# Performance work log

Hardware: AMD Instinct MI355X
Metric: run time of the kernel (lower is better)

The kernel has to match this reference:

```python
import jax, jax.numpy as jnp
import numpy as np

B, T, HOR = 128, 512, 64
M, Q, DFF = 1, 5, 7
D_IN = DFF + M            # 8
H = 512                   # d_hidden
NL = 2                    # n_layers
G = 4 * H                 # gate dim


def _cell(x, h, c, w_ih, w_hh, b):
    # PyTorch LSTM cell: gates ordered i, f, g, o
    g = x @ w_ih.T + h @ w_hh.T + b
    i, f, gg, o = jnp.split(g, 4, axis=-1)
    c = jax.nn.sigmoid(f) * c + jax.nn.sigmoid(i) * jnp.tanh(gg)
    h = jax.nn.sigmoid(o) * jnp.tanh(c)
    return h, c


def _bidi_layer(xs, w_ih, w_hh, b):
    # xs: [T, B, Din]; w_ih: [2, 4H, Din]; returns concat outputs and final states
    bsz = xs.shape[1]
    h0 = jnp.zeros((bsz, H), xs.dtype)

    def run(dirn, reverse):
        def step(carry, xt):
            h, c = carry
            h, c = _cell(xt, h, c, w_ih[dirn], w_hh[dirn], b[dirn])
            return (h, c), h
        (hT, cT), ys = jax.lax.scan(step, (h0, h0), xs, reverse=reverse)
        return ys, hT, cT

    ys_f, hf, cf = run(0, False)
    ys_b, hb, cb = run(1, True)
    return jnp.concatenate([ys_f, ys_b], axis=-1), (hf, hb, cf, cb)


def setup_inputs() -> dict:
    key = jax.random.key(0)
    ks = iter(jax.random.split(key, 24))
    s = 0.05
    inp = {
        "X": jax.random.normal(next(ks), (B, T, D_IN), jnp.float32),
        "future_features": jax.random.normal(next(ks), (B, HOR, DFF), jnp.float32),
        "Y_teacher": jax.random.normal(next(ks), (B, HOR, M), jnp.float32),
        "horizon_span": HOR,
        "enc_w_ih_l0": s * jax.random.normal(next(ks), (2, G, D_IN), jnp.float32),
        "enc_w_hh_l0": s * jax.random.normal(next(ks), (2, G, H), jnp.float32),
        "enc_b_l0": s * jax.random.normal(next(ks), (2, G), jnp.float32),
        "enc_w_ih_l1": s * jax.random.normal(next(ks), (2, G, 2 * H), jnp.float32),
        "enc_w_hh_l1": s * jax.random.normal(next(ks), (2, G, H), jnp.float32),
        "enc_b_l1": s * jax.random.normal(next(ks), (2, G), jnp.float32),
        "dec_w_ih_l0": s * jax.random.normal(next(ks), (G, D_IN), jnp.float32),
        "dec_w_hh_l0": s * jax.random.normal(next(ks), (G, H), jnp.float32),
        "dec_b_l0": s * jax.random.normal(next(ks), (G,), jnp.float32),
        "dec_w_ih_l1": s * jax.random.normal(next(ks), (G, H), jnp.float32),
        "dec_w_hh_l1": s * jax.random.normal(next(ks), (G, H), jnp.float32),
        "dec_b_l1": s * jax.random.normal(next(ks), (G,), jnp.float32),
        "w_bidi_h": s * jax.random.normal(next(ks), (NL * H, 2 * NL * H), jnp.float32),
        "b_bidi_h": s * jax.random.normal(next(ks), (NL * H,), jnp.float32),
        "w_out": s * jax.random.normal(next(ks), (M * Q, H), jnp.float32),
        "b_out": s * jax.random.normal(next(ks), (M * Q,), jnp.float32),
    }
    return inp


def reference(X, future_features, Y_teacher, horizon_span,
              enc_w_ih_l0, enc_w_hh_l0, enc_b_l0,
              enc_w_ih_l1, enc_w_hh_l1, enc_b_l1,
              dec_w_ih_l0, dec_w_hh_l0, dec_b_l0,
              dec_w_ih_l1, dec_w_hh_l1, dec_b_l1,
              w_bidi_h, b_bidi_h, w_out, b_out):
    bsz = X.shape[0]
    xs = jnp.swapaxes(X, 0, 1)  # [T, B, D_IN]

    ys1, (hf0, hb0, cf0, cb0) = _bidi_layer(xs, enc_w_ih_l0, enc_w_hh_l0, enc_b_l0)
    _,   (hf1, hb1, cf1, cb1) = _bidi_layer(ys1, enc_w_ih_l1, enc_w_hh_l1, enc_b_l1)

    # merge bidirectional final states: layout [B, (layer0 fwd|bwd, layer1 fwd|bwd)]
    h_flat = jnp.concatenate([hf0, hb0, hf1, hb1], axis=-1)  # [B, 2*NL*H]
    c_flat = jnp.concatenate([cf0, cb0, cf1, cb1], axis=-1)
    # NOTE: original module (faithfully) uses the *h* projection + ELU for c too
    h_m = jax.nn.elu(h_flat @ w_bidi_h.T + b_bidi_h).reshape(bsz, NL, H)
    c_m = jax.nn.elu(c_flat @ w_bidi_h.T + b_bidi_h).reshape(bsz, NL, H)

    futs = jnp.swapaxes(future_features, 0, 1)  # [HOR, B, DFF]
    inp_y0 = X[:, -1, :M]                        # [B, M]

    def step(carry, f_t):
        inp_y, h0, c0, h1, c1 = carry
        x = jnp.concatenate([inp_y, f_t], axis=-1)          # [B, D_IN]
        h0, c0 = _cell(x, h0, c0, dec_w_ih_l0, dec_w_hh_l0, dec_b_l0)
        h1, c1 = _cell(h0, h1, c1, dec_w_ih_l1, dec_w_hh_l1, dec_b_l1)
        y = h1 @ w_out.T + b_out                             # [B, M*Q]
        return (y[:, :M], h0, c0, h1, c1), y

    carry0 = (inp_y0, h_m[:, 0], c_m[:, 0], h_m[:, 1], c_m[:, 1])
    _, ys = jax.lax.scan(step, carry0, futs)                 # [HOR, B, M*Q]
    out = jnp.swapaxes(ys, 0, 1).reshape(bsz, horizon_span, M, Q)
    return out
```

## Files before the change

### kernel.cpp

```cpp
#include <hip/hip_runtime.h>
#include <hip/hip_bf16.h>
#include <cstddef>
#include <cstdint>


typedef __attribute__((ext_vector_type(8))) short short8;
typedef __attribute__((ext_vector_type(4))) float f32x4;

__device__ __forceinline__ float sigm_(float x) { return 1.0f / (1.0f + __expf(-x)); }

struct MProb {
  const __hip_bfloat16* A;
  const float* bpk;
  const __hip_bfloat16* S0;
  const __hip_bfloat16* S1;
  const float* cin;
  float* cout;
  __hip_bfloat16* hT;
  float* hf32;
  int ld0, ld1, ldh;
};

template<int N0, int N1, int KT, bool FIRST, bool WF32>
__global__ __launch_bounds__(256) void k_mcell(MProb P0, MProb P1)
{
  const MProb P = (blockIdx.x >= 32) ? P1 : P0;
  const int m0  = (blockIdx.x & 31) * 64;
  const int tid = threadIdx.x;
  const int lane = tid & 63;
  const int w  = tid >> 6;
  const int wm = w >> 1, wn = w & 1;
  const int r = lane & 15, q = lane >> 4;

  f32x4 acc[2][4];
#pragma unroll
  for (int am = 0; am < 2; ++am)
#pragma unroll
    for (int bn = 0; bn < 4; ++bn) acc[am][bn] = (f32x4){0.f, 0.f, 0.f, 0.f};

  const short* Ab = (const short*)P.A + (size_t)(m0 + wm * 32 + r) * KT + q * 8;

  if constexpr (!FIRST) {
    const short* Bb = (const short*)P.S0 + (size_t)(wn * 64 + r) * P.ld0 + q * 8;
    const size_t bs = (size_t)16 * P.ld0;
#pragma unroll 4
    for (int kk = 0; kk < N0; ++kk) {
      short8 a0 = *(const short8*)(Ab + kk * 32);
      short8 a1 = *(const short8*)(Ab + (size_t)16 * KT + kk * 32);
      short8 b0 = *(const short8*)(Bb + kk * 32);
      short8 b1 = *(const short8*)(Bb + kk * 32 + bs);
      short8 b2 = *(const short8*)(Bb + kk * 32 + 2 * bs);
      short8 b3 = *(const short8*)(Bb + kk * 32 + 3 * bs);
      acc[0][0] = __builtin_amdgcn_mfma_f32_16x16x32_bf16(a0, b0, acc[0][0], 0, 0, 0);
      acc[0][1] = __builtin_amdgcn_mfma_f32_16x16x32_bf16(a0, b1, acc[0][1], 0, 0, 0);
      acc[0][2] = __builtin_amdgcn_mfma_f32_16x16x32_bf16(a0, b2, acc[0][2], 0, 0, 0);
      acc[0][3] = __builtin_amdgcn_mfma_f32_16x16x32_bf16(a0, b3, acc[0][3], 0, 0, 0);
      acc[1][0] = __builtin_amdgcn_mfma_f32_16x16x32_bf16(a1, b0, acc[1][0], 0, 0, 0);
      acc[1][1] = __builtin_amdgcn_mfma_f32_16x16x32_bf16(a1, b1, acc[1][1], 0, 0, 0);
      acc[1][2] = __builtin_amdgcn_mfma_f32_16x16x32_bf16(a1, b2, acc[1][2], 0, 0, 0);
      acc[1][3] = __builtin_amdgcn_mfma_f32_16x16x32_bf16(a1, b3, acc[1][3], 0, 0, 0);
    }
  }
  {
    const short* Bb = (const short*)P.S1 + (size_t)(wn * 64 + r) * P.ld1 + q * 8;
    const size_t bs = (size_t)16 * P.ld1;
#pragma unroll 4
    for (int kk = 0; kk < N1; ++kk) {
      short8 a0 = *(const short8*)(Ab + (size_t)(N0 + kk) * 32);
      short8 a1 = *(const short8*)(Ab + (size_t)16 * KT + (size_t)(N0 + kk) * 32);
      short8 b0 = *(const short8*)(Bb + kk * 32);
      short8 b1 = *(const short8*)(Bb + kk * 32 + bs);
      short8 b2 = *(const short8*)(Bb + kk * 32 + 2 * bs);
      short8 b3 = *(const short8*)(Bb + kk * 32 + 3 * bs);
      acc[0][0] = __builtin_amdgcn_mfma_f32_16x16x32_bf16(a0, b0, acc[0][0], 0, 0, 0);
      acc[0][1] = __builtin_amdgcn_mfma_f32_16x16x32_bf16(a0, b1, acc[0][1], 0, 0, 0);
      acc[0][2] = __builtin_amdgcn_mfma_f32_16x16x32_bf16(a0, b2, acc[0][2], 0, 0, 0);
      acc[0][3] = __builtin_amdgcn_mfma_f32_16x16x32_bf16(a0, b3, acc[0][3], 0, 0, 0);
      acc[1][0] = __builtin_amdgcn_mfma_f32_16x16x32_bf16(a1, b0, acc[1][0], 0, 0, 0);
      acc[1][1] = __builtin_amdgcn_mfma_f32_16x16x32_bf16(a1, b1, acc[1][1], 0, 0, 0);
      acc[1][2] = __builtin_amdgcn_mfma_f32_16x16x32_bf16(a1, b2, acc[1][2], 0, 0, 0);
      acc[1][3] = __builtin_amdgcn_mfma_f32_16x16x32_bf16(a1, b3, acc[1][3], 0, 0, 0);
    }
  }

#pragma unroll
  for (int am = 0; am < 2; ++am) {
    const int pb = m0 + wm * 32 + am * 16 + q * 4;
    const int h  = pb >> 2;
    const float4 bb = *(const float4*)&P.bpk[pb];
#pragma unroll
    for (int bn = 0; bn < 4; ++bn) {
      const int col = wn * 64 + bn * 16 + r;
      float gi = acc[am][bn][0] + bb.x;
      float gf = acc[am][bn][1] + bb.y;
      float gg = acc[am][bn][2] + bb.z;
      float go = acc[am][bn][3] + bb.w;
      float cp = 0.0f;
      if constexpr (!FIRST) cp = P.cin[h * 128 + col];
      float c  = sigm_(gf) * cp + sigm_(gi) * tanhf(gg);
      float hv = sigm_(go) * tanhf(c);
      P.cout[h * 128 + col] = c;
      P.hT[(size_t)col * P.ldh + h] = __float2bfloat16(hv);
      if constexpr (WF32) P.hf32[h * 128 + col] = hv;
    }
  }
}

__global__ __launch_bounds__(256) void k_wpack(
    const float* __restrict__ Whh, const float* __restrict__ Wih,
    int XW, int KT, __hip_bfloat16* __restrict__ dst)
{
  int kc = blockIdx.x * 256 + threadIdx.x;
  int p  = blockIdx.y;
  if (kc >= KT) return;
  int h = p >> 2, g = p & 3;
  int row = g * 512 + h;
  float v;
  if (kc < 512)            v = Whh[(size_t)row * 512 + kc];
  else if (kc - 512 < XW)  v = Wih[(size_t)row * XW + (kc - 512)];
  else                     v = 0.0f;
  dst[(size_t)p * KT + kc] = __float2bfloat16(v);
}

__global__ __launch_bounds__(256) void k_bpack(
    const float* b0, const float* b1, const float* b2,
    const float* b3, const float* b4, const float* b5, float* bpk)
{
  int i = blockIdx.x * 256 + threadIdx.x;
  if (i >= 6 * 2048) return;
  int set = i >> 11, p = i & 2047;
  const float* src = set == 0 ? b0 : set == 1 ? b1 : set == 2 ? b2
                   : set == 3 ? b3 : set == 4 ? b4 : b5;
  bpk[i] = src[(p & 3) * 512 + (p >> 2)];
}

__global__ __launch_bounds__(256) void k_pre(
    const float* __restrict__ X, const float* __restrict__ fut,
    __hip_bfloat16* __restrict__ xpT, __hip_bfloat16* __restrict__ xdecTb)
{
  int t = blockIdx.x, tid = threadIdx.x;
  for (int i = tid; i < 4096; i += 256) {
    int b = i >> 5, j = i & 31;
    float v = (j < 8) ? X[(size_t)b * 4096 + t * 8 + j] : 0.0f;
    xpT[(size_t)t * 4096 + i] = __float2bfloat16(v);
  }
  if (t == 0 && tid < 128) {
    int b = tid;
    xdecTb[b * 32 + 0] = __float2bfloat16(X[(size_t)b * 4096 + 511 * 8 + 0]);
#pragma unroll
    for (int j = 0; j < 7; ++j)
      xdecTb[b * 32 + 1 + j] = __float2bfloat16(fut[(size_t)b * 448 + j]);
    for (int j = 8; j < 32; ++j) xdecTb[b * 32 + j] = __float2bfloat16(0.0f);
  }
}

__global__ __launch_bounds__(256) void k_mix(
    const float* __restrict__ h0f, const float* __restrict__ h0b,
    const float* __restrict__ h1f, const float* __restrict__ h1b,
    const float* __restrict__ c0f, const float* __restrict__ c0bb,
    const float* __restrict__ c1f, const float* __restrict__ c1bb,
    const float* __restrict__ w, const float* __restrict__ bias,
    float* __restrict__ h_dst, float* __restrict__ c_dst)
{
  int wgl  = blockIdx.x * 4 + (threadIdx.x >> 6);
  int lane = threadIdx.x & 63;
  int sel  = __builtin_amdgcn_readfirstlane(wgl >> 11);
  int rem  = wgl & 2047;
  int n    = __builtin_amdgcn_readfirstlane(rem >> 1);
  int half = rem & 1;
  int b    = (half << 6) + lane;
  const float* __restrict__ A0 = sel ? c0f  : h0f;
  const float* __restrict__ A1 = sel ? c0bb : h0b;
  const float* __restrict__ A2 = sel ? c1f  : h1f;
  const float* __restrict__ A3 = sel ? c1bb : h1b;
  const float* __restrict__ Wn = w + (size_t)n * 2048;
  float acc = bias[n];
#pragma unroll 8
  for (int k = 0; k < 512; ++k) acc = fmaf(A0[k * 128 + b], Wn[k], acc);
#pragma unroll 8
  for (int k = 0; k < 512; ++k) acc = fmaf(A1[k * 128 + b], Wn[512 + k], acc);
#pragma unroll 8
  for (int k = 0; k < 512; ++k) acc = fmaf(A2[k * 128 + b], Wn[1024 + k], acc);
#pragma unroll 8
  for (int k = 0; k < 512; ++k) acc = fmaf(A3[k * 128 + b], Wn[1536 + k], acc);
  float v = acc > 0.0f ? acc : (__expf(acc) - 1.0f);
  float* dst = sel ? c_dst : h_dst;
  dst[n * 128 + b] = v;
}

__global__ __launch_bounds__(256) void k_t2b(
    const float* __restrict__ hm, __hip_bfloat16* __restrict__ hdecT0)
{
  int i = blockIdx.x * 256 + threadIdx.x;
  if (i >= 131072) return;
  int n = i >> 7, b = i & 127;
  hdecT0[(size_t)(n >> 9) * 65536 + b * 512 + (n & 511)] = __float2bfloat16(hm[i]);
}

__global__ __launch_bounds__(256) void k_dec_out(
    const float* __restrict__ h1, const float* __restrict__ w_out,
    const float* __restrict__ b_out, const float* __restrict__ fut,
    float* __restrict__ out, __hip_bfloat16* __restrict__ xdecTb, int t)
{
  __shared__ float red[4][64];
  int bid = blockIdx.x;
  int tid = threadIdx.x;
  if (bid == 10) {
    if (tid < 128 && t + 1 < 64) {
      int b = tid;
#pragma unroll
      for (int j = 0; j < 7; ++j)
        xdecTb[b * 32 + 1 + j] = __float2bfloat16(fut[(size_t)b * 448 + (t + 1) * 7 + j]);
    }
    return;
  }
  int lane = tid & 63, warp = tid >> 6;
  int q    = __builtin_amdgcn_readfirstlane(bid >> 1);
  int half = bid & 1;
  int b    = half * 64 + lane;
  const float* __restrict__ Wq = w_out + q * 512 + warp * 128;
  const float* __restrict__ Hh = h1 + (size_t)warp * 128 * 128;
  float acc = 0.0f;
#pragma unroll 8
  for (int k = 0; k < 128; ++k) acc = fmaf(Hh[k * 128 + b], Wq[k], acc);
  red[warp][lane] = acc;
  __syncthreads();
  if (warp == 0) {
    float s = red[0][lane] + red[1][lane] + red[2][lane] + red[3][lane] + b_out[q];
    out[(size_t)b * 320 + t * 5 + q] = s;
    if (q == 0 && t + 1 < 64) xdecTb[b * 32] = __float2bfloat16(s);
  }
}

extern "C" void kernel_launch(void* const* d_in, const int* in_sizes, int n_in,
                              void* d_out, int out_size, void* d_ws, size_t ws_size,
                              hipStream_t stream) {
  (void)in_sizes; (void)n_in; (void)out_size; (void)ws_size;
  const float* X      = (const float*)d_in[0];
  const float* fut    = (const float*)d_in[1];
  const float* e_wih0 = (const float*)d_in[4];
  const float* e_whh0 = (const float*)d_in[5];
  const float* e_b0   = (const float*)d_in[6];
  const float* e_wih1 = (const float*)d_in[7];
  const float* e_whh1 = (const float*)d_in[8];
  const float* e_b1   = (const float*)d_in[9];
  const float* d_wih0 = (const float*)d_in[10];
  const float* d_whh0 = (const float*)d_in[11];
  const float* d_b0   = (const float*)d_in[12];
  const float* d_wih1 = (const float*)d_in[13];
  const float* d_whh1 = (const float*)d_in[14];
  const float* d_b1   = (const float*)d_in[15];
  const float* w_bidi = (const float*)d_in[16];
  const float* b_bidi = (const float*)d_in[17];
  const float* w_out  = (const float*)d_in[18];
  const float* b_out  = (const float*)d_in[19];
  float* out = (float*)d_out;

  float* ws = (float*)d_ws;
  __hip_bfloat16* xpT    = (__hip_bfloat16*)(ws + 0);
  __hip_bfloat16* ys1T   = (__hip_bfloat16*)(ws + 1048576);
  __hip_bfloat16* h1T    = (__hip_bfloat16*)(ws + 34603008);
  __hip_bfloat16* hdecT  = (__hip_bfloat16*)(ws + 34734080);
  __hip_bfloat16* xdecTb = (__hip_bfloat16*)(ws + 34865152);
  __hip_bfloat16* ApkL0  = (__hip_bfloat16*)(ws + 34867200);
  __hip_bfloat16* ApkL1  = (__hip_bfloat16*)(ws + 35981312);
  __hip_bfloat16* ApkD0  = (__hip_bfloat16*)(ws + 39127040);
  __hip_bfloat16* ApkD1  = (__hip_bfloat16*)(ws + 39684096);
  float* bpk   = ws + 40732672;
  float* hfin0 = ws + 40744960;
  float* hfin1 = ws + 40876032;
  float* c0buf = ws + 41007104;
  float* c1buf = ws + 41138176;
  float* cdec  = ws + 41269248;
  float* hmds  = ws + 41400320;
  float* hdecF = ws + 41531392;

  k_pre<<<512, 256, 0, stream>>>(X, fut, xpT, xdecTb);
  k_wpack<<<dim3(3, 2048), 256, 0, stream>>>(e_whh0, e_wih0, 8, 544, ApkL0);
  k_wpack<<<dim3(3, 2048), 256, 0, stream>>>(e_whh0 + (size_t)2048 * 512,
                                             e_wih0 + 2048 * 8, 8, 544,
                                             ApkL0 + (size_t)2048 * 544);
  k_wpack<<<dim3(6, 2048), 256, 0, stream>>>(e_whh1, e_wih1, 1024, 1536, ApkL1);
  k_wpack<<<dim3(6, 2048), 256, 0, stream>>>(e_whh1 + (size_t)2048 * 512,
                                             e_wih1 + (size_t)2048 * 1024, 1024, 1536,
                                             ApkL1 + (size_t)2048 * 1536);
  k_wpack<<<dim3(3, 2048), 256, 0, stream>>>(d_whh0, d_wih0, 8, 544, ApkD0);
  k_wpack<<<dim3(4, 2048), 256, 0, stream>>>(d_wih1, d_whh1, 512, 1024, ApkD1);
  k_bpack<<<48, 256, 0, stream>>>(e_b0, e_b0 + 2048, e_b1, e_b1 + 2048,
                                  d_b0, d_b1, bpk);

  for (int s = 0; s < 512; ++s) {
    int t = 511 - s;
    MProb P0{ApkL0, bpk, ys1T + (size_t)(s > 0 ? s - 1 : 0) * 131072,
             xpT + (size_t)s * 4096, c0buf, c0buf,
             ys1T + (size_t)s * 131072, hfin0, 1024, 32, 1024};
    MProb P1{ApkL0 + (size_t)2048 * 544, bpk + 2048,
             ys1T + (size_t)(512 - s) * 131072 + 512,
             xpT + (size_t)t * 4096, c0buf + 65536, c0buf + 65536,
             ys1T + (size_t)t * 131072 + 512, hfin0 + 65536, 1024, 32, 1024};
    if (s == 0) k_mcell<16, 1, 544, true,  true><<<64, 256, 0, stream>>>(P0, P1);
    else        k_mcell<16, 1, 544, false, true><<<64, 256, 0, stream>>>(P0, P1);
  }

  for (int s = 0; s < 512; ++s) {
    int t = 511 - s;
    int pr = s & 1, pw = pr ^ 1;
    MProb P0{ApkL1, bpk + 2 * 2048, h1T + (size_t)pr * 131072,
             ys1T + (size_t)s * 131072, c1buf, c1buf,
             h1T + (size_t)pw * 131072, hfin1, 512, 1024, 512};
    MProb P1{ApkL1 + (size_t)2048 * 1536, bpk + 3 * 2048,
             h1T + (size_t)pr * 131072 + 65536,
             ys1T + (size_t)t * 131072, c1buf + 65536, c1buf + 65536,
             h1T + (size_t)pw * 131072 + 65536, hfin1 + 65536, 512, 1024, 512};
    if (s == 0) k_mcell<16, 32, 1536, true,  true><<<64, 256, 0, stream>>>(P0, P1);
    else        k_mcell<16, 32, 1536, false, true><<<64, 256, 0, stream>>>(P0, P1);
  }

  k_mix<<<1024, 256, 0, stream>>>(
      hfin0, hfin0 + 65536, hfin1, hfin1 + 65536,
      c0buf, c0buf + 65536, c1buf, c1buf + 65536,
      w_bidi, b_bidi, hmds, cdec);
  k_t2b<<<512, 256, 0, stream>>>(hmds, hdecT);

  for (int t = 0; t < 64; ++t) {
    int pr = t & 1, pw = pr ^ 1;
    {
      MProb P0{ApkD0, bpk + 4 * 2048, hdecT + (size_t)pr * 131072,
               xdecTb, cdec, cdec,
               hdecT + (size_t)pw * 131072, nullptr, 512, 32, 512};
      k_mcell<16, 1, 544, false, false><<<32, 256, 0, stream>>>(P0, P0);
    }
    {
      MProb P0{ApkD1, bpk + 5 * 2048, hdecT + (size_t)pw * 131072,
               hdecT + (size_t)pr * 131072 + 65536, cdec + 65536, cdec + 65536,
               hdecT + (size_t)pw * 131072 + 65536, hdecF, 512, 512, 512};
      k_mcell<16, 16, 1024, false, true><<<32, 256, 0, stream>>>(P0, P0);
    }
    k_dec_out<<<11, 256, 0, stream>>>(hdecF, w_out, b_out, fut, out, xdecTb, t);
  }
}
```

Baseline: 30.46 ms.

## Replace per-step kernel launches with one persistent kernel using global barriers

Merges the per-timestep LSTM cell launches (about 1,200 launches over the encoder and decoder), the mix projection and the decoder output stages into a single persistent kernel of 128 blocks. Timesteps are separated by hand-rolled atomic grid barriers instead of kernel boundaries. The cell state now stays in registers across steps rather than going through global memory. Cross-block reads use system-scope atomic loads for coherence. This removes launch overhead and the cell-state round trips, but adds spin-barrier latency, relies on all 128 blocks being co-resident, and uses less-efficient uncached loads.

```diff
diff --git a/kernel.cpp b/kernel.cpp
--- a/kernel.cpp
+++ b/kernel.cpp
@@ -7,119 +7,271 @@
 typedef __attribute__((ext_vector_type(8))) short short8;
 typedef __attribute__((ext_vector_type(4))) float f32x4;
 
-__device__ __forceinline__ float sigm_(float x) { return 1.0f / (1.0f + __expf(-x)); }
-
-struct MProb {
-  const __hip_bfloat16* A;
-  const float* bpk;
-  const __hip_bfloat16* S0;
-  const __hip_bfloat16* S1;
-  const float* cin;
-  float* cout;
-  __hip_bfloat16* hT;
-  float* hf32;
-  int ld0, ld1, ldh;
+__device__ __forceinline__ float sigm_(float x){ return 1.0f/(1.0f+__expf(-x)); }
+
+__device__ __forceinline__ short bf16b(float x){
+  __hip_bfloat16 h = __float2bfloat16(x);
+  union { __hip_bfloat16 h; short s; } u; u.h = h; return u.s;
+}
+
+__device__ __forceinline__ short8 ld_sys8(const short* p){
+  union { unsigned long long u[2]; short8 s; } cv;
+  cv.u[0] = __hip_atomic_load((const unsigned long long*)p,     __ATOMIC_RELAXED, __HIP_MEMORY_SCOPE_SYSTEM);
+  cv.u[1] = __hip_atomic_load(((const unsigned long long*)p)+1, __ATOMIC_RELAXED, __HIP_MEMORY_SCOPE_SYSTEM);
+  return cv.s;
+}
+__device__ __forceinline__ float ld_sysf(const float* p){
+  unsigned u = __hip_atomic_load((const unsigned*)p, __ATOMIC_RELAXED, __HIP_MEMORY_SCOPE_SYSTEM);
+  union { unsigned u; float f; } c; c.u = u; return c.f;
+}
+
+template<int KN, bool SYS>
+__device__ __forceinline__ void gseg(const short* __restrict__ Ap,
+                                     const short* __restrict__ S, int ld,
+                                     int colr, int q, int a_k32_off,
+                                     f32x4 (&acc)[4])
+{
+#pragma unroll 4
+  for (int k32 = 0; k32 < KN; ++k32) {
+    short8 a = *(const short8*)(Ap + (size_t)(a_k32_off + k32) * 32);
+#pragma unroll
+    for (int bn = 0; bn < 4; ++bn) {
+      const short* bp = S + (size_t)(colr + bn * 16) * ld + k32 * 32 + q * 8;
+      short8 b;
+      if constexpr (SYS) b = ld_sys8(bp); else b = *(const short8*)bp;
+      acc[bn] = __builtin_amdgcn_mfma_f32_16x16x32_bf16(a, b, acc[bn], 0, 0, 0);
+    }
+  }
+}
+
+__device__ __forceinline__ void gbar(unsigned* base, int seq, int gbid, int nleaf)
+{
+  __syncthreads();
+  if (threadIdx.x == 0) {
+    unsigned* bb = base + (size_t)seq * 16;
+    unsigned prev = __hip_atomic_fetch_add(bb + (gbid >> 4), 1u, __ATOMIC_RELEASE, __HIP_MEMORY_SCOPE_SYSTEM);
+    if (prev == 15u)
+      __hip_atomic_fetch_add(bb + 15, 1u, __ATOMIC_RELEASE, __HIP_MEMORY_SCOPE_SYSTEM);
+    while (__hip_atomic_load(bb + 15, __ATOMIC_RELAXED, __HIP_MEMORY_SCOPE_SYSTEM) < (unsigned)nleaf)
+      __builtin_amdgcn_s_sleep(1);
+  }
+  __syncthreads();
+}
+
+struct PK {
+  const short *AL0, *AL1, *AD0, *AD1;
+  const float *bpk;
+  short *ys1T;
+  short *xpT;
+  short *h1T;
+  short *hdecT;
+  short *xdecTb;
+  float *hfin0, *hfin1, *cfin0, *cfin1;
+  float *cdec;
+  float *hdecF;
+  const float *wbidi, *bbidi, *wout, *bout, *fut;
+  float *out;
+  unsigned *barF, *barB, *barFull, *barD;
 };
 
-template<int N0, int N1, int KT, bool FIRST, bool WF32>
-__global__ __launch_bounds__(256) void k_mcell(MProb P0, MProb P1)
-{
-  const MProb P = (blockIdx.x >= 32) ? P1 : P0;
-  const int m0  = (blockIdx.x & 31) * 64;
-  const int tid = threadIdx.x;
+__global__ __launch_bounds__(256) void k_perst(PK P)
+{
+  __shared__ float red[4][64];
+  const int bid  = blockIdx.x;
+  const int tid  = threadIdx.x;
   const int lane = tid & 63;
-  const int w  = tid >> 6;
-  const int wm = w >> 1, wn = w & 1;
-  const int r = lane & 15, q = lane >> 4;
-
-  f32x4 acc[2][4];
-#pragma unroll
-  for (int am = 0; am < 2; ++am)
-#pragma unroll
-    for (int bn = 0; bn < 4; ++bn) acc[am][bn] = (f32x4){0.f, 0.f, 0.f, 0.f};
-
-  const short* Ab = (const short*)P.A + (size_t)(m0 + wm * 32 + r) * KT + q * 8;
-
-  if constexpr (!FIRST) {
-    const short* Bb = (const short*)P.S0 + (size_t)(wn * 64 + r) * P.ld0 + q * 8;
-    const size_t bs = (size_t)16 * P.ld0;
-#pragma unroll 4
-    for (int kk = 0; kk < N0; ++kk) {
-      short8 a0 = *(const short8*)(Ab + kk * 32);
-      short8 a1 = *(const short8*)(Ab + (size_t)16 * KT + kk * 32);
-      short8 b0 = *(const short8*)(Bb + kk * 32);
-      short8 b1 = *(const short8*)(Bb + kk * 32 + bs);
-      short8 b2 = *(const short8*)(Bb + kk * 32 + 2 * bs);
-      short8 b3 = *(const short8*)(Bb + kk * 32 + 3 * bs);
-      acc[0][0] = __builtin_amdgcn_mfma_f32_16x16x32_bf16(a0, b0, acc[0][0], 0, 0, 0);
-      acc[0][1] = __builtin_amdgcn_mfma_f32_16x16x32_bf16(a0, b1, acc[0][1], 0, 0, 0);
-      acc[0][2] = __builtin_amdgcn_mfma_f32_16x16x32_bf16(a0, b2, acc[0][2], 0, 0, 0);
-      acc[0][3] = __builtin_amdgcn_mfma_f32_16x16x32_bf16(a0, b3, acc[0][3], 0, 0, 0);
-      acc[1][0] = __builtin_amdgcn_mfma_f32_16x16x32_bf16(a1, b0, acc[1][0], 0, 0, 0);
-      acc[1][1] = __builtin_amdgcn_mfma_f32_16x16x32_bf16(a1, b1, acc[1][1], 0, 0, 0);
-      acc[1][2] = __builtin_amdgcn_mfma_f32_16x16x32_bf16(a1, b2, acc[1][2], 0, 0, 0);
-      acc[1][3] = __builtin_amdgcn_mfma_f32_16x16x32_bf16(a1, b3, acc[1][3], 0, 0, 0);
-    }
-  }
+  const int w    = tid >> 6;
+  const int r    = lane & 15, q = lane >> 4;
+  const int dir  = bid >> 6;
+  const int task = (bid & 63) * 4 + w;
+  const int rt   = task >> 1, ct = task & 1;
+  const int colbase = ct * 64;
+  const int colr = colbase + r;
+  const int rowr = rt * 16 + r;
+  const int hg   = rt * 4 + q;
+  const int prow4 = rt * 16 + q * 4;
+  unsigned* barMy = dir ? P.barB : P.barF;
+
   {
-    const short* Bb = (const short*)P.S1 + (size_t)(wn * 64 + r) * P.ld1 + q * 8;
-    const size_t bs = (size_t)16 * P.ld1;
-#pragma unroll 4
-    for (int kk = 0; kk < N1; ++kk) {
-      short8 a0 = *(const short8*)(Ab + (size_t)(N0 + kk) * 32);
-      short8 a1 = *(const short8*)(Ab + (size_t)16 * KT + (size_t)(N0 + kk) * 32);
-      short8 b0 = *(const short8*)(Bb + kk * 32);
-      short8 b1 = *(const short8*)(Bb + kk * 32 + bs);
-      short8 b2 = *(const short8*)(Bb + kk * 32 + 2 * bs);
-      short8 b3 = *(const short8*)(Bb + kk * 32 + 3 * bs);
-      acc[0][0] = __builtin_amdgcn_mfma_f32_16x16x32_bf16(a0, b0, acc[0][0], 0, 0, 0);
-      acc[0][1] = __builtin_amdgcn_mfma_f32_16x16x32_bf16(a0, b1, acc[0][1], 0, 0, 0);
-      acc[0][2] = __builtin_amdgcn_mfma_f32_16x16x32_bf16(a0, b2, acc[0][2], 0, 0, 0);
-      acc[0][3] = __builtin_amdgcn_mfma_f32_16x16x32_bf16(a0, b3, acc[0][3], 0, 0, 0);
-      acc[1][0] = __builtin_amdgcn_mfma_f32_16x16x32_bf16(a1, b0, acc[1][0], 0, 0, 0);
-      acc[1][1] = __builtin_amdgcn_mfma_f32_16x16x32_bf16(a1, b1, acc[1][1], 0, 0, 0);
-      acc[1][2] = __builtin_amdgcn_mfma_f32_16x16x32_bf16(a1, b2, acc[1][2], 0, 0, 0);
-      acc[1][3] = __builtin_amdgcn_mfma_f32_16x16x32_bf16(a1, b3, acc[1][3], 0, 0, 0);
-    }
-  }
-
-#pragma unroll
-  for (int am = 0; am < 2; ++am) {
-    const int pb = m0 + wm * 32 + am * 16 + q * 4;
-    const int h  = pb >> 2;
-    const float4 bb = *(const float4*)&P.bpk[pb];
-#pragma unroll
-    for (int bn = 0; bn < 4; ++bn) {
-      const int col = wn * 64 + bn * 16 + r;
-      float gi = acc[am][bn][0] + bb.x;
-      float gf = acc[am][bn][1] + bb.y;
-      float gg = acc[am][bn][2] + bb.z;
-      float go = acc[am][bn][3] + bb.w;
-      float cp = 0.0f;
-      if constexpr (!FIRST) cp = P.cin[h * 128 + col];
-      float c  = sigm_(gf) * cp + sigm_(gi) * tanhf(gg);
-      float hv = sigm_(go) * tanhf(c);
-      P.cout[h * 128 + col] = c;
-      P.hT[(size_t)col * P.ldh + h] = __float2bfloat16(hv);
-      if constexpr (WF32) P.hf32[h * 128 + col] = hv;
-    }
+    const short* A = P.AL0 + (size_t)dir * 2048 * 640;
+    const float4 bv = *(const float4*)(P.bpk + dir * 2048 + prow4);
+    const short* Ap = A + (size_t)rowr * 640 + q * 8;
+    float c[4] = {0.f, 0.f, 0.f, 0.f};
+    for (int s = 0; s < 512; ++s) {
+      int t  = dir ? 511 - s : s;
+      int tp = dir ? 512 - s : s - 1;
+      f32x4 acc[4];
+#pragma unroll
+      for (int bn = 0; bn < 4; ++bn) acc[bn] = (f32x4){0.f,0.f,0.f,0.f};
+      if (s > 0)
+        gseg<16, false>(Ap, P.ys1T + (size_t)tp * 131072 + dir * 512, 1024, colr, q, 0, acc);
+      gseg<4, false>(Ap, P.xpT + (size_t)t * 16384, 128, colr, q, 16, acc);
+#pragma unroll
+      for (int bn = 0; bn < 4; ++bn) {
+        int col = colbase + bn * 16 + r;
+        float gi = acc[bn][0]+bv.x, gf = acc[bn][1]+bv.y, gg = acc[bn][2]+bv.z, go = acc[bn][3]+bv.w;
+        float cc = sigm_(gf)*c[bn] + sigm_(gi)*tanhf(gg);
+        float hv = sigm_(go)*tanhf(cc);
+        c[bn] = cc;
+        P.ys1T[(size_t)t * 131072 + (size_t)col * 1024 + dir * 512 + hg] = bf16b(hv);
+        if (s == 511) {
+          P.hfin0[(dir * 512 + hg) * 128 + col] = hv;
+          P.cfin0[(dir * 512 + hg) * 128 + col] = cc;
+        }
+      }
+      gbar(barMy, s, bid & 63, 4);
+    }
+  }
+  gbar(P.barFull, 0, bid, 8);
+
+  {
+    const short* A = P.AL1 + (size_t)dir * 2048 * 1536;
+    const float4 bv = *(const float4*)(P.bpk + (2 + dir) * 2048 + prow4);
+    const short* Ap = A + (size_t)rowr * 1536 + q * 8;
+    float c[4] = {0.f, 0.f, 0.f, 0.f};
+    for (int s = 0; s < 512; ++s) {
+      int t  = dir ? 511 - s : s;
+      int pr = s & 1, pw = pr ^ 1;
+      f32x4 acc[4];
+#pragma unroll
+      for (int bn = 0; bn < 4; ++bn) acc[bn] = (f32x4){0.f,0.f,0.f,0.f};
+      if (s > 0)
+        gseg<16, true>(Ap, P.h1T + (size_t)(pr * 2 + dir) * 65536, 512, colr, q, 0, acc);
+      gseg<32, false>(Ap, P.ys1T + (size_t)t * 131072, 1024, colr, q, 16, acc);
+#pragma unroll
+      for (int bn = 0; bn < 4; ++bn) {
+        int col = colbase + bn * 16 + r;
+        float gi = acc[bn][0]+bv.x, gf = acc[bn][1]+bv.y, gg = acc[bn][2]+bv.z, go = acc[bn][3]+bv.w;
+        float cc = sigm_(gf)*c[bn] + sigm_(gi)*tanhf(gg);
+        float hv = sigm_(go)*tanhf(cc);
+        c[bn] = cc;
+        P.h1T[(size_t)(pw * 2 + dir) * 65536 + (size_t)col * 512 + hg] = bf16b(hv);
+        if (s == 511) {
+          P.hfin1[(dir * 512 + hg) * 128 + col] = hv;
+          P.cfin1[(dir * 512 + hg) * 128 + col] = cc;
+        }
+      }
+      gbar(barMy, 512 + s, bid & 63, 4);
+    }
+  }
+  gbar(P.barFull, 1, bid, 8);
+
+  {
+    int gid = bid * 4 + w;
+    for (int it = 0; it < 8; ++it) {
+      int wgl = gid * 8 + it;
+      int sel = wgl >> 11, rem = wgl & 2047, n = rem >> 1, half = rem & 1;
+      int b = half * 64 + lane;
+      const float* A0 = sel ? P.cfin0 : P.hfin0;
+      const float* A2 = sel ? P.cfin1 : P.hfin1;
+      const float* Wn = P.wbidi + (size_t)n * 2048;
+      float a = P.bbidi[n];
+#pragma unroll 8
+      for (int k = 0; k < 512; ++k) a = fmaf(A0[k * 128 + b], Wn[k], a);
+#pragma unroll 8
+      for (int k = 0; k < 512; ++k) a = fmaf(A0[65536 + k * 128 + b], Wn[512 + k], a);
+#pragma unroll 8
+      for (int k = 0; k < 512; ++k) a = fmaf(A2[k * 128 + b], Wn[1024 + k], a);
+#pragma unroll 8
+      for (int k = 0; k < 512; ++k) a = fmaf(A2[65536 + k * 128 + b], Wn[1536 + k], a);
+      float v = a > 0.f ? a : (__expf(a) - 1.f);
+      if (sel == 0)
+        P.hdecT[(size_t)(n >> 9) * 65536 + (size_t)b * 512 + (n & 511)] = bf16b(v);
+      else
+        P.cdec[(size_t)(n >> 9) * 65536 + (size_t)(n & 511) * 128 + b] = v;
+    }
+  }
+  gbar(P.barFull, 2, bid, 8);
+
+  if (bid >= 64) return;
+
+  float cL0[4], cL1[4];
+#pragma unroll
+  for (int bn = 0; bn < 4; ++bn) {
+    int col = colbase + bn * 16 + r;
+    cL0[bn] = P.cdec[hg * 128 + col];
+    cL1[bn] = P.cdec[65536 + hg * 128 + col];
+  }
+  const float4 bv0 = *(const float4*)(P.bpk + 4 * 2048 + prow4);
+  const float4 bv1 = *(const float4*)(P.bpk + 5 * 2048 + prow4);
+  const short* Ap0 = P.AD0 + (size_t)rowr * 640 + q * 8;
+  const short* Ap1 = P.AD1 + (size_t)rowr * 1024 + q * 8;
+
+  for (int t = 0; t < 64; ++t) {
+    int pr = t & 1, pw = pr ^ 1;
+    {
+      f32x4 acc[4];
+#pragma unroll
+      for (int bn = 0; bn < 4; ++bn) acc[bn] = (f32x4){0.f,0.f,0.f,0.f};
+      gseg<16, true>(Ap0, P.hdecT + (size_t)(pr * 2 + 0) * 65536, 512, colr, q, 0, acc);
+      gseg<4,  true>(Ap0, P.xdecTb, 128, colr, q, 16, acc);
+#pragma unroll
+      for (int bn = 0; bn < 4; ++bn) {
+        int col = colbase + bn * 16 + r;
+        float gi = acc[bn][0]+bv0.x, gf = acc[bn][1]+bv0.y, gg = acc[bn][2]+bv0.z, go = acc[bn][3]+bv0.w;
+        float cc = sigm_(gf)*cL0[bn] + sigm_(gi)*tanhf(gg);
+        float hv = sigm_(go)*tanhf(cc);
+        cL0[bn] = cc;
+        P.hdecT[(size_t)(pw * 2 + 0) * 65536 + (size_t)col * 512 + hg] = bf16b(hv);
+      }
+      gbar(P.barD, t * 3 + 0, bid, 4);
+    }
+    {
+      f32x4 acc[4];
+#pragma unroll
+      for (int bn = 0; bn < 4; ++bn) acc[bn] = (f32x4){0.f,0.f,0.f,0.f};
+      gseg<16, true>(Ap1, P.hdecT + (size_t)(pw * 2 + 0) * 65536, 512, colr, q, 0, acc);
+      gseg<16, true>(Ap1, P.hdecT + (size_t)(pr * 2 + 1) * 65536, 512, colr, q, 16, acc);
+#pragma unroll
+      for (int bn = 0; bn < 4; ++bn) {
+        int col = colbase + bn * 16 + r;
+        float gi = acc[bn][0]+bv1.x, gf = acc[bn][1]+bv1.y, gg = acc[bn][2]+bv1.z, go = acc[bn][3]+bv1.w;
+        float cc = sigm_(gf)*cL1[bn] + sigm_(gi)*tanhf(gg);
+        float hv = sigm_(go)*tanhf(cc);
+        cL1[bn] = cc;
+        P.hdecT[(size_t)(pw * 2 + 1) * 65536 + (size_t)col * 512 + hg] = bf16b(hv);
+        P.hdecF[hg * 128 + col] = hv;
+      }
+      gbar(P.barD, t * 3 + 1, bid, 4);
+    }
+    if (bid < 10) {
+      int qq = bid >> 1, half = bid & 1;
+      int b = half * 64 + lane;
+      const float* Wq = P.wout + qq * 512 + w * 128;
+      float a = 0.f;
+#pragma unroll 8
+      for (int k = 0; k < 128; ++k)
+        a = fmaf(ld_sysf(P.hdecF + (size_t)(w * 128 + k) * 128 + b), Wq[k], a);
+      red[w][lane] = a;
+      __syncthreads();
+      if (w == 0) {
+        float y = red[0][lane] + red[1][lane] + red[2][lane] + red[3][lane] + P.bout[qq];
+        P.out[(size_t)b * 320 + t * 5 + qq] = y;
+        if (qq == 0 && t + 1 < 64) P.xdecTb[(size_t)b * 128] = bf16b(y);
+      }
+    } else if (bid == 10 && t + 1 < 64) {
+      for (int i = tid; i < 896; i += 256) {
+        int b = i / 7, j = i % 7;
+        P.xdecTb[(size_t)b * 128 + 1 + j] = bf16b(P.fut[(size_t)b * 448 + (t + 1) * 7 + j]);
+      }
+    }
+    gbar(P.barD, t * 3 + 2, bid, 4);
   }
 }
 
 __global__ __launch_bounds__(256) void k_wpack(
     const float* __restrict__ Whh, const float* __restrict__ Wih,
-    int XW, int KT, __hip_bfloat16* __restrict__ dst)
+    int XW, int KT, short* __restrict__ dst)
 {
   int kc = blockIdx.x * 256 + threadIdx.x;
   int p  = blockIdx.y;
   if (kc >= KT) return;
-  int h = p >> 2, g = p & 3;
-  int row = g * 512 + h;
+  int row = (p & 3) * 512 + (p >> 2);
   float v;
-  if (kc < 512)            v = Whh[(size_t)row * 512 + kc];
-  else if (kc - 512 < XW)  v = Wih[(size_t)row * XW + (kc - 512)];
-  else                     v = 0.0f;
-  dst[(size_t)p * KT + kc] = __float2bfloat16(v);
+  if (kc < 512)           v = Whh[(size_t)row * 512 + kc];
+  else if (kc - 512 < XW) v = Wih[(size_t)row * XW + (kc - 512)];
+  else                    v = 0.0f;
+  dst[(size_t)p * KT + kc] = bf16b(v);
 }
 
 __global__ __launch_bounds__(256) void k_bpack(
@@ -136,99 +288,23 @@
 
 __global__ __launch_bounds__(256) void k_pre(
     const float* __restrict__ X, const float* __restrict__ fut,
-    __hip_bfloat16* __restrict__ xpT, __hip_bfloat16* __restrict__ xdecTb)
+    short* __restrict__ xpT, short* __restrict__ xdecTb)
 {
   int t = blockIdx.x, tid = threadIdx.x;
-  for (int i = tid; i < 4096; i += 256) {
-    int b = i >> 5, j = i & 31;
+  for (int i = tid; i < 16384; i += 256) {
+    int b = i >> 7, j = i & 127;
     float v = (j < 8) ? X[(size_t)b * 4096 + t * 8 + j] : 0.0f;
-    xpT[(size_t)t * 4096 + i] = __float2bfloat16(v);
-  }
-  if (t == 0 && tid < 128) {
-    int b = tid;
-    xdecTb[b * 32 + 0] = __float2bfloat16(X[(size_t)b * 4096 + 511 * 8 + 0]);
-#pragma unroll
-    for (int j = 0; j < 7; ++j)
-      xdecTb[b * 32 + 1 + j] = __float2bfloat16(fut[(size_t)b * 448 + j]);
-    for (int j = 8; j < 32; ++j) xdecTb[b * 32 + j] = __float2bfloat16(0.0f);
-  }
-}
-
-__global__ __launch_bounds__(256) void k_mix(
-    const float* __restrict__ h0f, const float* __restrict__ h0b,
-    const float* __restrict__ h1f, const float* __restrict__ h1b,
-    const float* __restrict__ c0f, const float* __restrict__ c0bb,
-    const float* __restrict__ c1f, const float* __restrict__ c1bb,
-    const float* __restrict__ w, const float* __restrict__ bias,
-    float* __restrict__ h_dst, float* __restrict__ c_dst)
-{
-  int wgl  = blockIdx.x * 4 + (threadIdx.x >> 6);
-  int lane = threadIdx.x & 63;
-  int sel  = __builtin_amdgcn_readfirstlane(wgl >> 11);
-  int rem  = wgl & 2047;
-  int n    = __builtin_amdgcn_readfirstlane(rem >> 1);
-  int half = rem & 1;
-  int b    = (half << 6) + lane;
-  const float* __restrict__ A0 = sel ? c0f  : h0f;
-  const float* __restrict__ A1 = sel ? c0bb : h0b;
-  const float* __restrict__ A2 = sel ? c1f  : h1f;
-  const float* __restrict__ A3 = sel ? c1bb : h1b;
-  const float* __restrict__ Wn = w + (size_t)n * 2048;
-  float acc = bias[n];
-#pragma unroll 8
-  for (int k = 0; k < 512; ++k) acc = fmaf(A0[k * 128 + b], Wn[k], acc);
-#pragma unroll 8
-  for (int k = 0; k < 512; ++k) acc = fmaf(A1[k * 128 + b], Wn[512 + k], acc);
-#pragma unroll 8
-  for (int k = 0; k < 512; ++k) acc = fmaf(A2[k * 128 + b], Wn[1024 + k], acc);
-#pragma unroll 8
-  for (int k = 0; k < 512; ++k) acc = fmaf(A3[k * 128 + b], Wn[1536 + k], acc);
-  float v = acc > 0.0f ? acc : (__expf(acc) - 1.0f);
-  float* dst = sel ? c_dst : h_dst;
-  dst[n * 128 + b] = v;
-}
-
-__global__ __launch_bounds__(256) void k_t2b(
-    const float* __restrict__ hm, __hip_bfloat16* __restrict__ hdecT0)
-{
-  int i = blockIdx.x * 256 + threadIdx.x;
-  if (i >= 131072) return;
-  int n = i >> 7, b = i & 127;
-  hdecT0[(size_t)(n >> 9) * 65536 + b * 512 + (n & 511)] = __float2bfloat16(hm[i]);
-}
-
-__global__ __launch_bounds__(256) void k_dec_out(
-    const float* __restrict__ h1, const float* __restrict__ w_out,
-    const float* __restrict__ b_out, const float* __restrict__ fut,
-    float* __restrict__ out, __hip_bfloat16* __restrict__ xdecTb, int t)
-{
-  __shared__ float red[4][64];
-  int bid = blockIdx.x;
-  int tid = threadIdx.x;
-  if (bid == 10) {
-    if (tid < 128 && t + 1 < 64) {
-      int b = tid;
-#pragma unroll
-      for (int j = 0; j < 7; ++j)
-        xdecTb[b * 32 + 1 + j] = __float2bfloat16(fut[(size_t)b * 448 + (t + 1) * 7 + j]);
-    }
-    return;
-  }
-  int lane = tid & 63, warp = tid >> 6;
-  int q    = __builtin_amdgcn_readfirstlane(bid >> 1);
-  int half = bid & 1;
-  int b    = half * 64 + lane;
-  const float* __restrict__ Wq = w_out + q * 512 + warp * 128;
-  const float* __restrict__ Hh = h1 + (size_t)warp * 128 * 128;
-  float acc = 0.0f;
-#pragma unroll 8
-  for (int k = 0; k < 128; ++k) acc = fmaf(Hh[k * 128 + b], Wq[k], acc);
-  red[warp][lane] = acc;
-  __syncthreads();
-  if (warp == 0) {
-    float s = red[0][lane] + red[1][lane] + red[2][lane] + red[3][lane] + b_out[q];
-    out[(size_t)b * 320 + t * 5 + q] = s;
-    if (q == 0 && t + 1 < 64) xdecTb[b * 32] = __float2bfloat16(s);
+    xpT[(size_t)t * 16384 + i] = bf16b(v);
+  }
+  if (t == 0) {
+    for (int i = tid; i < 16384; i += 256) {
+      int b = i >> 7, j = i & 127;
+      float v;
+      if (j == 0)     v = X[(size_t)b * 4096 + 511 * 8 + 0];
+      else if (j < 8) v = fut[(size_t)b * 448 + (j - 1)];
+      else            v = 0.0f;
+      xdecTb[i] = bf16b(v);
+    }
   }
 }
 
@@ -257,85 +333,52 @@
   float* out = (float*)d_out;
 
   float* ws = (float*)d_ws;
-  __hip_bfloat16* xpT    = (__hip_bfloat16*)(ws + 0);
-  __hip_bfloat16* ys1T   = (__hip_bfloat16*)(ws + 1048576);
-  __hip_bfloat16* h1T    = (__hip_bfloat16*)(ws + 34603008);
-  __hip_bfloat16* hdecT  = (__hip_bfloat16*)(ws + 34734080);
-  __hip_bfloat16* xdecTb = (__hip_bfloat16*)(ws + 34865152);
-  __hip_bfloat16* ApkL0  = (__hip_bfloat16*)(ws + 34867200);
-  __hip_bfloat16* ApkL1  = (__hip_bfloat16*)(ws + 35981312);
-  __hip_bfloat16* ApkD0  = (__hip_bfloat16*)(ws + 39127040);
-  __hip_bfloat16* ApkD1  = (__hip_bfloat16*)(ws + 39684096);
-  float* bpk   = ws + 40732672;
-  float* hfin0 = ws + 40744960;
-  float* hfin1 = ws + 40876032;
-  float* c0buf = ws + 41007104;
-  float* c1buf = ws + 41138176;
-  float* cdec  = ws + 41269248;
-  float* hmds  = ws + 41400320;
-  float* hdecF = ws + 41531392;
-
+  short* ys1T   = (short*)(ws + 0);
+  short* xpT    = (short*)(ws + 33554432);
+  short* h1T    = (short*)(ws + 37748736);
+  short* hdecT  = (short*)(ws + 37879808);
+  short* xdecTb = (short*)(ws + 38010880);
+  short* ApkL0  = (short*)(ws + 38019072);
+  short* ApkL1  = (short*)(ws + 39329792);
+  short* ApkD0  = (short*)(ws + 42475520);
+  short* ApkD1  = (short*)(ws + 43130880);
+  float* bpk    = ws + 44179456;
+  float* hfin0  = ws + 44191744;
+  float* hfin1  = ws + 44322816;
+  float* cfin0  = ws + 44453888;
+  float* cfin1  = ws + 44584960;
+  float* cdec   = ws + 44716032;
+  float* hdecF  = ws + 44847104;
+  unsigned* bars = (unsigned*)(ws + 44912640);
+  unsigned* barF    = bars;
+  unsigned* barB    = barF + 1024 * 16;
+  unsigned* barFull = barB + 1024 * 16;
+  unsigned* barD    = barFull + 4 * 16;
+
+  hipMemsetAsync(bars, 0, (size_t)36864 * 4, stream);
   k_pre<<<512, 256, 0, stream>>>(X, fut, xpT, xdecTb);
-  k_wpack<<<dim3(3, 2048), 256, 0, stream>>>(e_whh0, e_wih0, 8, 544, ApkL0);
+  k_wpack<<<dim3(3, 2048), 256, 0, stream>>>(e_whh0, e_wih0, 8, 640, ApkL0);
   k_wpack<<<dim3(3, 2048), 256, 0, stream>>>(e_whh0 + (size_t)2048 * 512,
-                                             e_wih0 + 2048 * 8, 8, 544,
-                                             ApkL0 + (size_t)2048 * 544);
+                                             e_wih0 + 2048 * 8, 8, 640,
+                                             ApkL0 + (size_t)2048 * 640);
   k_wpack<<<dim3(6, 2048), 256, 0, stream>>>(e_whh1, e_wih1, 1024, 1536, ApkL1);
   k_wpack<<<dim3(6, 2048), 256, 0, stream>>>(e_whh1 + (size_t)2048 * 512,
                                              e_wih1 + (size_t)2048 * 1024, 1024, 1536,
                                              ApkL1 + (size_t)2048 * 1536);
-  k_wpack<<<dim3(3, 2048), 256, 0, stream>>>(d_whh0, d_wih0, 8, 544, ApkD0);
+  k_wpack<<<dim3(3, 2048), 256, 0, stream>>>(d_whh0, d_wih0, 8, 640, ApkD0);
   k_wpack<<<dim3(4, 2048), 256, 0, stream>>>(d_wih1, d_whh1, 512, 1024, ApkD1);
   k_bpack<<<48, 256, 0, stream>>>(e_b0, e_b0 + 2048, e_b1, e_b1 + 2048,
                                   d_b0, d_b1, bpk);
 
-  for (int s = 0; s < 512; ++s) {
-    int t = 511 - s;
-    MProb P0{ApkL0, bpk, ys1T + (size_t)(s > 0 ? s - 1 : 0) * 131072,
-             xpT + (size_t)s * 4096, c0buf, c0buf,
-             ys1T + (size_t)s * 131072, hfin0, 1024, 32, 1024};
-    MProb P1{ApkL0 + (size_t)2048 * 544, bpk + 2048,
-             ys1T + (size_t)(512 - s) * 131072 + 512,
-             xpT + (size_t)t * 4096, c0buf + 65536, c0buf + 65536,
-             ys1T + (size_t)t * 131072 + 512, hfin0 + 65536, 1024, 32, 1024};
-    if (s == 0) k_mcell<16, 1, 544, true,  true><<<64, 256, 0, stream>>>(P0, P1);
-    else        k_mcell<16, 1, 544, false, true><<<64, 256, 0, stream>>>(P0, P1);
-  }
-
-  for (int s = 0; s < 512; ++s) {
-    int t = 511 - s;
-    int pr = s & 1, pw = pr ^ 1;
-    MProb P0{ApkL1, bpk + 2 * 2048, h1T + (size_t)pr * 131072,
-             ys1T + (size_t)s * 131072, c1buf, c1buf,
-             h1T + (size_t)pw * 131072, hfin1, 512, 1024, 512};
-    MProb P1{ApkL1 + (size_t)2048 * 1536, bpk + 3 * 2048,
-             h1T + (size_t)pr * 131072 + 65536,
-             ys1T + (size_t)t * 131072, c1buf + 65536, c1buf + 65536,
-             h1T + (size_t)pw * 131072 + 65536, hfin1 + 65536, 512, 1024, 512};
-    if (s == 0) k_mcell<16, 32, 1536, true,  true><<<64, 256, 0, stream>>>(P0, P1);
-    else        k_mcell<16, 32, 1536, false, true><<<64, 256, 0, stream>>>(P0, P1);
-  }
-
-  k_mix<<<1024, 256, 0, stream>>>(
-      hfin0, hfin0 + 65536, hfin1, hfin1 + 65536,
-      c0buf, c0buf + 65536, c1buf, c1buf + 65536,
-      w_bidi, b_bidi, hmds, cdec);
-  k_t2b<<<512, 256, 0, stream>>>(hmds, hdecT);
-
-  for (int t = 0; t < 64; ++t) {
-    int pr = t & 1, pw = pr ^ 1;
-    {
-      MProb P0{ApkD0, bpk + 4 * 2048, hdecT + (size_t)pr * 131072,
-               xdecTb, cdec, cdec,
-               hdecT + (size_t)pw * 131072, nullptr, 512, 32, 512};
-      k_mcell<16, 1, 544, false, false><<<32, 256, 0, stream>>>(P0, P0);
-    }
-    {
-      MProb P0{ApkD1, bpk + 5 * 2048, hdecT + (size_t)pw * 131072,
-               hdecT + (size_t)pr * 131072 + 65536, cdec + 65536, cdec + 65536,
-               hdecT + (size_t)pw * 131072 + 65536, hdecF, 512, 512, 512};
-      k_mcell<16, 16, 1024, false, true><<<32, 256, 0, stream>>>(P0, P0);
-    }
-    k_dec_out<<<11, 256, 0, stream>>>(hdecF, w_out, b_out, fut, out, xdecTb, t);
-  }
-}
+  PK P;
+  P.AL0 = ApkL0; P.AL1 = ApkL1; P.AD0 = ApkD0; P.AD1 = ApkD1;
+  P.bpk = bpk;
+  P.ys1T = ys1T; P.xpT = xpT; P.h1T = h1T; P.hdecT = hdecT; P.xdecTb = xdecTb;
+  P.hfin0 = hfin0; P.hfin1 = hfin1; P.cfin0 = cfin0; P.cfin1 = cfin1;
+  P.cdec = cdec; P.hdecF = hdecF;
+  P.wbidi = w_bidi; P.bbidi = b_bidi; P.wout = w_out; P.bout = b_out; P.fut = fut;
+  P.out = out;
+  P.barF = barF; P.barB = barB; P.barFull = barFull; P.barD = barD;
+
+  k_perst<<<128, 256, 0, stream>>>(P);
+}
```

New measurement: 42.23 ms. 38.6% more time.
